# Kernel optimization log

Hardware: AMD Instinct MI355X
Metric: run time of the kernel (lower is better)

Reference implementation:

```python
import jax, jax.numpy as jnp
import numpy as np

N_NODES = 50000
N_EDGES = 800000
N_GRAPHS = 128
HEADS = 4
HDIM = 32
N_CLASSES = 10
LEAKY_ALPHA = 0.2


def setup_inputs() -> dict:
    key = jax.random.key(0)
    ks = jax.random.split(key, 12)
    src = jax.random.randint(ks[0], (N_EDGES,), 0, N_NODES, dtype=jnp.int32)
    # guarantee every node has in-degree >= 1 so 3/deg is finite
    dst_tail = jax.random.randint(ks[1], (N_EDGES - N_NODES,), 0, N_NODES, dtype=jnp.int32)
    dst = jnp.concatenate([jnp.arange(N_NODES, dtype=jnp.int32), dst_tail])
    graph_ids = jnp.sort(jax.random.randint(ks[2], (N_NODES,), 0, N_GRAPHS, dtype=jnp.int32))
    s = 0.1
    return {
        "src": src,
        "dst": dst,
        "graph_ids": graph_ids,
        "W1": jax.random.normal(ks[3], (4, HEADS * HDIM), jnp.float32) * s,
        "al1": jax.random.normal(ks[4], (HEADS, HDIM), jnp.float32) * s,
        "ar1": jax.random.normal(ks[5], (HEADS, HDIM), jnp.float32) * s,
        "W2": jax.random.normal(ks[6], (HEADS * HDIM, HEADS * HDIM), jnp.float32) * s,
        "al2": jax.random.normal(ks[7], (HEADS, HDIM), jnp.float32) * s,
        "ar2": jax.random.normal(ks[8], (HEADS, HDIM), jnp.float32) * s,
        "Wc": jax.random.normal(ks[9], (HEADS * HDIM, N_CLASSES), jnp.float32) * s,
        "bc": jax.random.normal(ks[10], (N_CLASSES,), jnp.float32) * s,
    }


def _gat_layer(x, src, dst, W, al, ar):
    # x: [N, Fin]; W: [Fin, H*D]; al, ar: [H, D]
    n = x.shape[0]
    ft = (x @ W).reshape(n, HEADS, HDIM)                       # [N, H, D]
    a1 = jnp.einsum("nhd,hd->nh", ft, al)                      # [N, H]
    a2 = jnp.einsum("nhd,hd->nh", ft, ar)                      # [N, H]
    e = jax.nn.leaky_relu(a1[src] + a2[dst], LEAKY_ALPHA)      # [E, H]
    # segment softmax over incoming edges of each dst node
    m = jax.ops.segment_max(e, dst, num_segments=n)            # [N, H]
    m = jax.lax.stop_gradient(m)
    ex = jnp.exp(e - m[dst])                                   # [E, H]
    denom = jax.ops.segment_sum(ex, dst, num_segments=n)       # [N, H]
    alpha = ex / denom[dst]                                    # [E, H]
    # gather-multiply-scatter aggregation
    out = jax.ops.segment_sum(ft[src] * alpha[:, :, None], dst, num_segments=n)  # [N, H, D]
    return jax.nn.relu(out.reshape(n, HEADS * HDIM))


def reference(src, dst, graph_ids, W1, al1, ar1, W2, al2, ar2, Wc, bc):
    n = N_NODES
    ones_e = jnp.ones(src.shape[0], jnp.float32)
    deg = jax.ops.segment_sum(ones_e, dst, num_segments=n)     # in-degrees [N]
    h = jnp.stack(
        [deg, (deg - 3.0 > 0).astype(jnp.float32), 3.0 / deg, (deg - 4.0 > 0).astype(jnp.float32)],
        axis=1,
    )                                                          # [N, 4]
    h = _gat_layer(h, src, dst, W1, al1, ar1)                  # [N, H*D]
    h = _gat_layer(h, src, dst, W2, al2, ar2)                  # [N, H*D]
    # mean_nodes: per-graph mean pooling
    gsum = jax.ops.segment_sum(h, graph_ids, num_segments=N_GRAPHS)
    cnt = jax.ops.segment_sum(jnp.ones(n, jnp.float32), graph_ids, num_segments=N_GRAPHS)
    gmean = gsum / jnp.maximum(cnt, 1.0)[:, None]              # [G, H*D]
    return jax.nn.sigmoid(gmean @ Wc + bc)                     # [G, n_classes]
```

## Files before the change

kernel.cpp:

```cpp
#include <hip/hip_runtime.h>
#include <hip/hip_fp16.h>
#include <math.h>

#define HEADS 4
#define HDIM 32
#define FDIM 128
#define NGRAPH 128
#define NCLASS 10

#define NBW 128
#define NBP 512
#define BCAP 4096
#define SLICE 4096

typedef _Float16 h4_t __attribute__((ext_vector_type(4)));
typedef float f4_t __attribute__((ext_vector_type(4)));
typedef float f2_t __attribute__((ext_vector_type(2)));

__device__ __forceinline__ float lrelu(float x) { return fmaxf(x, 0.2f * x); }

__global__ void k_wfrag(const float* __restrict__ W2, __half* __restrict__ Wfrag,
                        float* __restrict__ gsum, int* __restrict__ gcnt,
                        int* __restrict__ bcur) {
    int gid = blockIdx.x * 256 + threadIdx.x;
    ((float4*)gsum)[gid] = make_float4(0.f, 0.f, 0.f, 0.f);
    if (gid < NGRAPH) gcnt[gid] = 0;
    if (gid < NBP) bcur[gid] = 0;
    int fid = gid >> 6, l = gid & 63;
    int ks = fid >> 3, t = fid & 7;
    int k0 = ks * 16 + 4 * (l >> 4);
    int n0 = t * 16 + (l & 15);
    __half2 lo = __floats2half2_rn(W2[(k0 + 0) * FDIM + n0], W2[(k0 + 1) * FDIM + n0]);
    __half2 hi = __floats2half2_rn(W2[(k0 + 2) * FDIM + n0], W2[(k0 + 3) * FDIM + n0]);
    size_t base = ((size_t)fid * 64 + l) * 4;
    *(__half2*)(Wfrag + base)     = lo;
    *(__half2*)(Wfrag + base + 2) = hi;
}

__global__ __launch_bounds__(256) void k_part(const int* __restrict__ src,
        const int* __restrict__ dst, int E, int* __restrict__ bcur,
        unsigned int* __restrict__ part) {
    __shared__ int lcnt[NBP];
    __shared__ int loff[NBP];
    __shared__ int lpos[NBP];
    __shared__ unsigned int staged[SLICE];
    __shared__ int tgt[SLICE];
    __shared__ int ws[4];
    int tid = threadIdx.x, lane = tid & 63, w = tid >> 6;
    int beg = blockIdx.x * SLICE, end = min(E, beg + SLICE);
    int m = end - beg;
    for (int i = tid; i < NBP; i += 256) lcnt[i] = 0;
    __syncthreads();
    for (int i = beg + tid; i < end; i += 256)
        atomicAdd(&lcnt[dst[i] >> 7], 1);
    __syncthreads();
    int c0 = lcnt[2 * tid], c1 = lcnt[2 * tid + 1];
    int t = c0 + c1;
    int incl = t;
    #pragma unroll
    for (int off = 1; off < 64; off <<= 1) {
        int y = __shfl_up(incl, off);
        if (lane >= off) incl += y;
    }
    if (lane == 63) ws[w] = incl;
    __syncthreads();
    int wpre = 0;
    #pragma unroll
    for (int j = 0; j < 4; ++j) if (j < w) wpre += ws[j];
    int ex = wpre + (incl - t);
    loff[2 * tid] = ex; loff[2 * tid + 1] = ex + c0;
    if (c0) lpos[2 * tid] = atomicAdd(&bcur[2 * tid], c0);
    if (c1) lpos[2 * tid + 1] = atomicAdd(&bcur[2 * tid + 1], c1);
    lcnt[2 * tid] = 0; lcnt[2 * tid + 1] = 0;
    __syncthreads();
    for (int i = beg + tid; i < end; i += 256) {
        int s = src[i], d = dst[i];
        int b = d >> 7;
        int idx = atomicAdd(&lcnt[b], 1);
        int slot = loff[b] + idx;
        staged[slot] = ((unsigned int)(d & (NBW - 1)) << 16) | (unsigned int)s;
        tgt[slot] = b * BCAP + lpos[b] + idx;
    }
    __syncthreads();
    for (int i = tid; i < m; i += 256)
        part[tgt[i]] = staged[i];
}

__global__ __launch_bounds__(256) void k_build(const unsigned int* __restrict__ part,
        const int* __restrict__ bcur, unsigned int* __restrict__ nodeinfo,
        unsigned short* __restrict__ csr, unsigned short* __restrict__ deg16, int n) {
    __shared__ int ldeg[NBW];
    __shared__ int loffs[NBW];
    __shared__ int wtot[2];
    int b = blockIdx.x, tid = threadIdx.x;
    int lane = tid & 63, w = tid >> 6;
    if (tid < NBW) ldeg[tid] = 0;
    __syncthreads();
    int beg = b * BCAP, end = beg + bcur[b];
    for (int i = beg + tid; i < end; i += 256)
        atomicAdd(&ldeg[part[i] >> 16], 1);
    __syncthreads();
    int x = (tid < NBW) ? ldeg[tid] : 0;
    int incl = x;
    #pragma unroll
    for (int off = 1; off < 64; off <<= 1) {
        int y = __shfl_up(incl, off);
        if (lane >= off) incl += y;
    }
    if (tid < NBW && lane == 63) wtot[w] = incl;
    __syncthreads();
    if (tid < NBW) {
        int pre = incl - x;
        if (w == 1) pre += wtot[0];
        loffs[tid] = beg + pre;
        int v = b * NBW + tid;
        if (v < n) {
            nodeinfo[v] = ((unsigned int)(beg + pre) << 9) | (unsigned int)x;
            deg16[v] = (unsigned short)x;
        }
    }
    __syncthreads();
    if (tid < NBW) ldeg[tid] = 0;
    __syncthreads();
    for (int i = beg + tid; i < end; i += 256) {
        unsigned int e = part[i];
        int lv = e >> 16;
        int p = atomicAdd(&ldeg[lv], 1);
        csr[loffs[lv] + p] = (unsigned short)(e & 0xffffu);
    }
}

__global__ __launch_bounds__(256) void k_l2f(const unsigned int* __restrict__ nodeinfo,
        const unsigned short* __restrict__ csr, const unsigned short* __restrict__ deg16,
        const float* __restrict__ W1, const float* __restrict__ al1,
        const float* __restrict__ ar1, const __half* __restrict__ Wfrag,
        const float* __restrict__ al, const float* __restrict__ ar,
        unsigned char* __restrict__ ft8, float* __restrict__ a1b,
        float* __restrict__ a2b, int n) {
    __shared__ __half Alds[4][16 * 132];
    __shared__ float Slds[4][256];
    __shared__ float wla[16], wlr[16];
    int tid = threadIdx.x, l = tid & 63, w = tid >> 6;
    int c = l & 15, g = l >> 4;

    if (tid < 32) {
        int k = (tid & 15) >> 2, h = tid & 3;
        const float* av = (tid < 16) ? al1 : ar1;
        float s = 0.f;
        #pragma unroll
        for (int d = 0; d < 32; ++d) s += W1[k * FDIM + h * HDIM + d] * av[h * HDIM + d];
        if (tid < 16) wla[k * 4 + h] = s; else wlr[k * 4 + h] = s;
    }
    __syncthreads();

    int v0 = (blockIdx.x * 4 + w) * 16;

    for (int r4 = 0; r4 < 4; ++r4) {
        int v = v0 + r4 * 4 + g;
        bool vok = v < n;
        unsigned int info = vok ? nodeinfo[v] : 0;
        int beg = info >> 9;
        int dg = info & 511;
        float dv = vok ? (float)dg : 1.0f;
        float4 hvv = make_float4(dv, (dv - 3.0f > 0.0f) ? 1.0f : 0.0f, 3.0f / dv,
                                 (dv - 4.0f > 0.0f) ? 1.0f : 0.0f);
        float a2h[4];
        #pragma unroll
        for (int h = 0; h < 4; ++h)
            a2h[h] = hvv.x * wlr[0 + h] + hvv.y * wlr[4 + h] + hvv.z * wlr[8 + h] + hvv.w * wlr[12 + h];
        float P[4][4], D[4];
        #pragma unroll
        for (int h = 0; h < 4; ++h) { D[h] = 0.f;
            #pragma unroll
            for (int d = 0; d < 4; ++d) P[h][d] = 0.f; }
        for (int base2 = 0; base2 < dg; base2 += 16) {
            if (base2 + c < dg) {
                int u = csr[beg + base2 + c];
                float du = (float)deg16[u];
                float4 fu = make_float4(du, (du - 3.0f > 0.0f) ? 1.0f : 0.0f, 3.0f / du,
                                        (du - 4.0f > 0.0f) ? 1.0f : 0.0f);
                float wgt[4];
                #pragma unroll
                for (int h = 0; h < 4; ++h) {
                    float a1h = fu.x * wla[0 + h] + fu.y * wla[4 + h] + fu.z * wla[8 + h] + fu.w * wla[12 + h];
                    wgt[h] = __expf(lrelu(a1h + a2h[h]));
                }
                #pragma unroll
                for (int h = 0; h < 4; ++h) {
                    D[h] += wgt[h];
                    P[h][0] = fmaf(wgt[h], fu.x, P[h][0]);
                    P[h][1] = fmaf(wgt[h], fu.y, P[h][1]);
                    P[h][2] = fmaf(wgt[h], fu.z, P[h][2]);
                    P[h][3] = fmaf(wgt[h], fu.w, P[h][3]);
                }
            }
        }
        #pragma unroll
        for (int off = 1; off < 16; off <<= 1) {
            #pragma unroll
            for (int h = 0; h < 4; ++h) {
                D[h] += __shfl_xor(D[h], off);
                #pragma unroll
                for (int d = 0; d < 4; ++d) P[h][d] += __shfl_xor(P[h][d], off);
            }
        }
        if (vok && c == 0) {
            #pragma unroll
            for (int h = 0; h < 4; ++h) {
                float r = 1.0f / D[h];
                #pragma unroll
                for (int d = 0; d < 4; ++d)
                    Slds[w][(r4 * 4 + g) * 16 + h * 4 + d] = P[h][d] * r;
            }
        }
    }

    float2 w1c[4];
    #pragma unroll
    for (int d = 0; d < 4; ++d) w1c[d] = *(const float2*)(W1 + d * FDIM + 2 * l);
    for (int jj = 0; jj < 16; ++jj) {
        float4 s = *(const float4*)(&Slds[w][jj * 16 + g * 4]);
        float t0 = s.x * w1c[0].x + s.y * w1c[1].x + s.z * w1c[2].x + s.w * w1c[3].x;
        float t1 = s.x * w1c[0].y + s.y * w1c[1].y + s.z * w1c[2].y + s.w * w1c[3].y;
        *(__half2*)(&Alds[w][jj * 132 + 2 * l]) = __floats2half2_rn(fmaxf(t0, 0.f), fmaxf(t1, 0.f));
    }
    __syncthreads();

    f4_t acc[8];
    #pragma unroll
    for (int t = 0; t < 8; ++t) acc[t] = (f4_t){0.f, 0.f, 0.f, 0.f};
    #pragma unroll
    for (int ks = 0; ks < 8; ++ks) {
        h4_t af = *(const h4_t*)(&Alds[w][c * 132 + ks * 16 + 4 * g]);
        #pragma unroll
        for (int t = 0; t < 8; ++t) {
            h4_t bf = *(const h4_t*)(Wfrag + ((size_t)(ks * 8 + t) * 64 + l) * 4);
            acc[t] = __builtin_amdgcn_mfma_f32_16x16x16f16(af, bf, acc[t], 0, 0, 0);
        }
    }

    #pragma unroll
    for (int t = 0; t < 8; ++t) {
        #pragma unroll
        for (int r = 0; r < 4; ++r) {
            int v = v0 + 4 * g + r;
            if (v < n) {
                int pk = __builtin_amdgcn_cvt_pk_fp8_f32(acc[t][r], acc[t][r], 0, false);
                ft8[(size_t)v * FDIM + t * 16 + c] = (unsigned char)(pk & 0xff);
            }
        }
    }
    float al0[4], al1v[4], ar0[4], ar1v[4];
    #pragma unroll
    for (int h = 0; h < 4; ++h) {
        al0[h] = al[h * 32 + c]; al1v[h] = al[h * 32 + 16 + c];
        ar0[h] = ar[h * 32 + c]; ar1v[h] = ar[h * 32 + 16 + c];
    }
    #pragma unroll
    for (int r = 0; r < 4; ++r) {
        int v = v0 + 4 * g + r;
        #pragma unroll
        for (int h = 0; h < 4; ++h) {
            float p1 = acc[2 * h][r] * al0[h] + acc[2 * h + 1][r] * al1v[h];
            float p2 = acc[2 * h][r] * ar0[h] + acc[2 * h + 1][r] * ar1v[h];
            #pragma unroll
            for (int off = 1; off < 16; off <<= 1) {
                p1 += __shfl_xor(p1, off);
                p2 += __shfl_xor(p2, off);
            }
            if (c == h && v < n) {
                a1b[v * 4 + h] = p1;
                a2b[v * 4 + h] = p2;
            }
        }
    }
}

__global__ __launch_bounds__(256) void k_agg2(const unsigned int* __restrict__ nodeinfo,
        const unsigned short* __restrict__ csr, const unsigned char* __restrict__ ft8,
        const float* __restrict__ a1, const float* __restrict__ a2,
        __half* __restrict__ out, int n) {
    int tid = threadIdx.x, lane = tid & 63, w = tid >> 6;
    int qw = lane >> 4, ql = lane & 15;
    int v = blockIdx.x * 16 + w * 4 + qw;
    if (v >= n) return;
    unsigned int info = nodeinfo[v];
    int beg = info >> 9, end = beg + (info & 511);
    int h = ql >> 2;
    float a2h = a2[v * 4 + h];
    float acc[8];
    #pragma unroll
    for (int k = 0; k < 8; ++k) acc[k] = 0.f;
    float dsum = 0.f;
    const unsigned char* fbase = ft8 + (size_t)ql * 8;
    int j = beg;
    for (; j + 4 <= end; j += 4) {
        int s[4];
        #pragma unroll
        for (int k = 0; k < 4; ++k) s[k] = csr[j + k];
        float wv[4]; uint2 bv[4];
        #pragma unroll
        for (int k = 0; k < 4; ++k) {
            wv[k] = __expf(lrelu(a1[s[k] * 4 + h] + a2h));
            bv[k] = *(const uint2*)(fbase + (size_t)s[k] * FDIM);
        }
        #pragma unroll
        for (int k = 0; k < 4; ++k) {
            dsum += wv[k];
            f2_t g;
            g = __builtin_amdgcn_cvt_pk_f32_fp8(bv[k].x, false); acc[0] = fmaf(wv[k], g[0], acc[0]); acc[1] = fmaf(wv[k], g[1], acc[1]);
            g = __builtin_amdgcn_cvt_pk_f32_fp8(bv[k].x, true);  acc[2] = fmaf(wv[k], g[0], acc[2]); acc[3] = fmaf(wv[k], g[1], acc[3]);
            g = __builtin_amdgcn_cvt_pk_f32_fp8(bv[k].y, false); acc[4] = fmaf(wv[k], g[0], acc[4]); acc[5] = fmaf(wv[k], g[1], acc[5]);
            g = __builtin_amdgcn_cvt_pk_f32_fp8(bv[k].y, true);  acc[6] = fmaf(wv[k], g[0], acc[6]); acc[7] = fmaf(wv[k], g[1], acc[7]);
        }
    }
    for (; j < end; ++j) {
        int s0 = csr[j];
        float w0 = __expf(lrelu(a1[s0 * 4 + h] + a2h));
        uint2 b0 = *(const uint2*)(fbase + (size_t)s0 * FDIM);
        dsum += w0;
        f2_t g;
        g = __builtin_amdgcn_cvt_pk_f32_fp8(b0.x, false); acc[0] = fmaf(w0, g[0], acc[0]); acc[1] = fmaf(w0, g[1], acc[1]);
        g = __builtin_amdgcn_cvt_pk_f32_fp8(b0.x, true);  acc[2] = fmaf(w0, g[0], acc[2]); acc[3] = fmaf(w0, g[1], acc[3]);
        g = __builtin_amdgcn_cvt_pk_f32_fp8(b0.y, false); acc[4] = fmaf(w0, g[0], acc[4]); acc[5] = fmaf(w0, g[1], acc[5]);
        g = __builtin_amdgcn_cvt_pk_f32_fp8(b0.y, true);  acc[6] = fmaf(w0, g[0], acc[6]); acc[7] = fmaf(w0, g[1], acc[7]);
    }
    float r = 1.0f / dsum;
    __half2 o[4];
    #pragma unroll
    for (int k = 0; k < 4; ++k)
        o[k] = __floats2half2_rn(fmaxf(acc[2 * k] * r, 0.f), fmaxf(acc[2 * k + 1] * r, 0.f));
    *(float4*)(out + (size_t)v * FDIM + ql * 8) = *(float4*)o;
}

__global__ void k_pool(const __half* __restrict__ hbuf, const int* __restrict__ gid,
                       float* __restrict__ gsum, int* __restrict__ gcnt, int n) {
    const int STRIP = 32;
    int wv = (blockIdx.x * blockDim.x + threadIdx.x) >> 6;
    int lane = threadIdx.x & 63;
    int beg = wv * STRIP;
    if (beg >= n) return;
    int end = min(beg + STRIP, n);
    int f = 2 * lane;
    float2 acc = make_float2(0.f, 0.f);
    int cur = gid[beg];
    int cnt = 0;
    for (int i = beg; i < end; ++i) {
        int g = gid[i];
        if (g != cur) {
            atomicAdd(&gsum[cur * FDIM + f], acc.x);
            atomicAdd(&gsum[cur * FDIM + f + 1], acc.y);
            if (lane == 0) atomicAdd(&gcnt[cur], cnt);
            acc = make_float2(0.f, 0.f); cnt = 0; cur = g;
        }
        float2 x = __half22float2(*(const __half2*)(hbuf + (size_t)i * FDIM + f));
        acc.x += x.x; acc.y += x.y; cnt++;
    }
    atomicAdd(&gsum[cur * FDIM + f], acc.x);
    atomicAdd(&gsum[cur * FDIM + f + 1], acc.y);
    if (lane == 0) atomicAdd(&gcnt[cur], cnt);
}

__global__ void k_classify(const float* __restrict__ gsum, const int* __restrict__ gcnt,
                           const float* __restrict__ Wc, const float* __restrict__ bc,
                           float* __restrict__ out) {
    int idx = blockIdx.x * blockDim.x + threadIdx.x;
    if (idx >= NGRAPH * NCLASS) return;
    int g = idx / NCLASS, c = idx % NCLASS;
    float rc = 1.0f / fmaxf((float)gcnt[g], 1.0f);
    float s = bc[c];
    for (int k = 0; k < FDIM; ++k)
        s += gsum[g * FDIM + k] * rc * Wc[k * NCLASS + c];
    out[idx] = 1.0f / (1.0f + __expf(-s));
}

extern "C" void kernel_launch(void* const* d_in, const int* in_sizes, int n_in,
                              void* d_out, int out_size, void* d_ws, size_t ws_size,
                              hipStream_t stream) {
    const int*   src = (const int*)d_in[0];
    const int*   dst = (const int*)d_in[1];
    const int*   gid = (const int*)d_in[2];
    const float* W1  = (const float*)d_in[3];
    const float* al1 = (const float*)d_in[4];
    const float* ar1 = (const float*)d_in[5];
    const float* W2  = (const float*)d_in[6];
    const float* al2 = (const float*)d_in[7];
    const float* ar2 = (const float*)d_in[8];
    const float* Wc  = (const float*)d_in[9];
    const float* bc  = (const float*)d_in[10];
    float* out = (float*)d_out;
    const int E = in_sizes[0];
    const int N = in_sizes[2];

    char* ws = (char*)d_ws;
    size_t off = 0;
    auto alloc = [&](size_t bytes) -> void* {
        void* p = ws + off;
        off = (off + bytes + 255) & ~(size_t)255;
        return p;
    };
    unsigned int*   part = (unsigned int*)alloc((size_t)NBP * BCAP * 4);
    unsigned short* csr  = (unsigned short*)alloc((size_t)NBP * BCAP * 2);
    int*    bcur   = (int*)alloc(NBP * 4);
    unsigned int* nodeinfo = (unsigned int*)alloc((size_t)N * 4);
    unsigned short* deg16  = (unsigned short*)alloc((size_t)N * 2);
    float*  a1b    = (float*)alloc((size_t)N * HEADS * 4);
    float*  a2b    = (float*)alloc((size_t)N * HEADS * 4);
    unsigned char* ft8 = (unsigned char*)alloc((size_t)N * FDIM);
    __half* hbuf   = (__half*)alloc((size_t)N * FDIM * 2);
    __half* Wfrag  = (__half*)alloc((size_t)FDIM * FDIM * 2);
    float*  gsum   = (float*)alloc((size_t)NGRAPH * FDIM * 4);
    int*    gcnt   = (int*)alloc((size_t)NGRAPH * 4);

    int pb_edges = (E + SLICE - 1) / SLICE;
    int nb2 = (N + NBW - 1) / NBW;

    k_wfrag<<<16, 256, 0, stream>>>(W2, Wfrag, gsum, gcnt, bcur);
    k_part<<<pb_edges, 256, 0, stream>>>(src, dst, E, bcur, part);
    k_build<<<nb2, 256, 0, stream>>>(part, bcur, nodeinfo, csr, deg16, N);
    k_l2f<<<(N + 63) / 64, 256, 0, stream>>>(nodeinfo, csr, deg16, W1, al1, ar1,
                                             Wfrag, al2, ar2, ft8, a1b, a2b, N);
    k_agg2<<<(N + 15) / 16, 256, 0, stream>>>(nodeinfo, csr, ft8, a1b, a2b, hbuf, N);

    int pb = (((N + 31) / 32) + 3) / 4;
    k_pool<<<pb, 256, 0, stream>>>(hbuf, gid, gsum, gcnt, N);
    k_classify<<<(NGRAPH * NCLASS + 255) / 256, 256, 0, stream>>>(gsum, gcnt, Wc, bc, out);
}
```

Before: 121.4 us.

## Split layer-1 aggregation into its own kernel with one node per 16-lane group

The fused layer-1 aggregation plus layer-2 MFMA projection kernel is split in two. The new aggregation kernel gives each 16-lane group a single node across more blocks, and writes the 16 normalized feature sums per node to a global buffer. The projection kernel then reads those sums instead of shared memory. This is meant to raise parallelism and occupancy for the irregular gather phase and free the MFMA kernel from serial per-node loops, at the cost of an extra launch and a round trip of 64 bytes per node through global memory.

```diff
diff --git a/kernel.cpp b/kernel.cpp
--- a/kernel.cpp
+++ b/kernel.cpp
@@ -130,96 +130,94 @@
     }
 }
 
-__global__ __launch_bounds__(256) void k_l2f(const unsigned int* __restrict__ nodeinfo,
+__global__ __launch_bounds__(256) void k_agg1(const unsigned int* __restrict__ nodeinfo,
         const unsigned short* __restrict__ csr, const unsigned short* __restrict__ deg16,
         const float* __restrict__ W1, const float* __restrict__ al1,
-        const float* __restrict__ ar1, const __half* __restrict__ Wfrag,
+        const float* __restrict__ ar1, float* __restrict__ Sbuf, int n) {
+    __shared__ float wla[16], wlr[16];
+    int tid = threadIdx.x;
+    if (tid < 32) {
+        int k = (tid & 15) >> 2, h = tid & 3;
+        const float* av = (tid < 16) ? al1 : ar1;
+        float s = 0.f;
+        #pragma unroll
+        for (int d = 0; d < 32; ++d) s += W1[k * FDIM + h * HDIM + d] * av[h * HDIM + d];
+        if (tid < 16) wla[k * 4 + h] = s; else wlr[k * 4 + h] = s;
+    }
+    __syncthreads();
+    int c = tid & 15;
+    int v = blockIdx.x * 16 + (tid >> 4);
+    if (v >= n) return;
+    unsigned int info = nodeinfo[v];
+    int beg = info >> 9;
+    int dg = info & 511;
+    float dv = (float)dg;
+    float4 hvv = make_float4(dv, (dv - 3.0f > 0.0f) ? 1.0f : 0.0f, 3.0f / dv,
+                             (dv - 4.0f > 0.0f) ? 1.0f : 0.0f);
+    float a2h[4];
+    #pragma unroll
+    for (int h = 0; h < 4; ++h)
+        a2h[h] = hvv.x * wlr[0 + h] + hvv.y * wlr[4 + h] + hvv.z * wlr[8 + h] + hvv.w * wlr[12 + h];
+    float P[4][4], D[4];
+    #pragma unroll
+    for (int h = 0; h < 4; ++h) { D[h] = 0.f;
+        #pragma unroll
+        for (int d = 0; d < 4; ++d) P[h][d] = 0.f; }
+    for (int j = beg + c; j < beg + dg; j += 16) {
+        int u = csr[j];
+        float du = (float)deg16[u];
+        float4 fu = make_float4(du, (du - 3.0f > 0.0f) ? 1.0f : 0.0f, 3.0f / du,
+                                (du - 4.0f > 0.0f) ? 1.0f : 0.0f);
+        float wgt[4];
+        #pragma unroll
+        for (int h = 0; h < 4; ++h) {
+            float a1h = fu.x * wla[0 + h] + fu.y * wla[4 + h] + fu.z * wla[8 + h] + fu.w * wla[12 + h];
+            wgt[h] = __expf(lrelu(a1h + a2h[h]));
+        }
+        #pragma unroll
+        for (int h = 0; h < 4; ++h) {
+            D[h] += wgt[h];
+            P[h][0] = fmaf(wgt[h], fu.x, P[h][0]);
+            P[h][1] = fmaf(wgt[h], fu.y, P[h][1]);
+            P[h][2] = fmaf(wgt[h], fu.z, P[h][2]);
+            P[h][3] = fmaf(wgt[h], fu.w, P[h][3]);
+        }
+    }
+    #pragma unroll
+    for (int off = 1; off < 16; off <<= 1) {
+        #pragma unroll
+        for (int h = 0; h < 4; ++h) {
+            D[h] += __shfl_xor(D[h], off);
+            #pragma unroll
+            for (int d = 0; d < 4; ++d) P[h][d] += __shfl_xor(P[h][d], off);
+        }
+    }
+    if (c == 0) {
+        #pragma unroll
+        for (int h = 0; h < 4; ++h) {
+            float r = 1.0f / D[h];
+            *(float4*)(Sbuf + v * 16 + h * 4) =
+                make_float4(P[h][0] * r, P[h][1] * r, P[h][2] * r, P[h][3] * r);
+        }
+    }
+}
+
+__global__ __launch_bounds__(256) void k_layer2(const float* __restrict__ Sbuf,
+        const float* __restrict__ W1, const __half* __restrict__ Wfrag,
         const float* __restrict__ al, const float* __restrict__ ar,
         unsigned char* __restrict__ ft8, float* __restrict__ a1b,
         float* __restrict__ a2b, int n) {
     __shared__ __half Alds[4][16 * 132];
-    __shared__ float Slds[4][256];
-    __shared__ float wla[16], wlr[16];
     int tid = threadIdx.x, l = tid & 63, w = tid >> 6;
     int c = l & 15, g = l >> 4;
-
-    if (tid < 32) {
-        int k = (tid & 15) >> 2, h = tid & 3;
-        const float* av = (tid < 16) ? al1 : ar1;
-        float s = 0.f;
-        #pragma unroll
-        for (int d = 0; d < 32; ++d) s += W1[k * FDIM + h * HDIM + d] * av[h * HDIM + d];
-        if (tid < 16) wla[k * 4 + h] = s; else wlr[k * 4 + h] = s;
-    }
-    __syncthreads();
-
     int v0 = (blockIdx.x * 4 + w) * 16;
-
-    for (int r4 = 0; r4 < 4; ++r4) {
-        int v = v0 + r4 * 4 + g;
-        bool vok = v < n;
-        unsigned int info = vok ? nodeinfo[v] : 0;
-        int beg = info >> 9;
-        int dg = info & 511;
-        float dv = vok ? (float)dg : 1.0f;
-        float4 hvv = make_float4(dv, (dv - 3.0f > 0.0f) ? 1.0f : 0.0f, 3.0f / dv,
-                                 (dv - 4.0f > 0.0f) ? 1.0f : 0.0f);
-        float a2h[4];
-        #pragma unroll
-        for (int h = 0; h < 4; ++h)
-            a2h[h] = hvv.x * wlr[0 + h] + hvv.y * wlr[4 + h] + hvv.z * wlr[8 + h] + hvv.w * wlr[12 + h];
-        float P[4][4], D[4];
-        #pragma unroll
-        for (int h = 0; h < 4; ++h) { D[h] = 0.f;
-            #pragma unroll
-            for (int d = 0; d < 4; ++d) P[h][d] = 0.f; }
-        for (int base2 = 0; base2 < dg; base2 += 16) {
-            if (base2 + c < dg) {
-                int u = csr[beg + base2 + c];
-                float du = (float)deg16[u];
-                float4 fu = make_float4(du, (du - 3.0f > 0.0f) ? 1.0f : 0.0f, 3.0f / du,
-                                        (du - 4.0f > 0.0f) ? 1.0f : 0.0f);
-                float wgt[4];
-                #pragma unroll
-                for (int h = 0; h < 4; ++h) {
-                    float a1h = fu.x * wla[0 + h] + fu.y * wla[4 + h] + fu.z * wla[8 + h] + fu.w * wla[12 + h];
-                    wgt[h] = __expf(lrelu(a1h + a2h[h]));
-                }
-                #pragma unroll
-                for (int h = 0; h < 4; ++h) {
-                    D[h] += wgt[h];
-                    P[h][0] = fmaf(wgt[h], fu.x, P[h][0]);
-                    P[h][1] = fmaf(wgt[h], fu.y, P[h][1]);
-                    P[h][2] = fmaf(wgt[h], fu.z, P[h][2]);
-                    P[h][3] = fmaf(wgt[h], fu.w, P[h][3]);
-                }
-            }
-        }
-        #pragma unroll
-        for (int off = 1; off < 16; off <<= 1) {
-            #pragma unroll
-            for (int h = 0; h < 4; ++h) {
-                D[h] += __shfl_xor(D[h], off);
-                #pragma unroll
-                for (int d = 0; d < 4; ++d) P[h][d] += __shfl_xor(P[h][d], off);
-            }
-        }
-        if (vok && c == 0) {
-            #pragma unroll
-            for (int h = 0; h < 4; ++h) {
-                float r = 1.0f / D[h];
-                #pragma unroll
-                for (int d = 0; d < 4; ++d)
-                    Slds[w][(r4 * 4 + g) * 16 + h * 4 + d] = P[h][d] * r;
-            }
-        }
-    }
 
     float2 w1c[4];
     #pragma unroll
     for (int d = 0; d < 4; ++d) w1c[d] = *(const float2*)(W1 + d * FDIM + 2 * l);
     for (int jj = 0; jj < 16; ++jj) {
-        float4 s = *(const float4*)(&Slds[w][jj * 16 + g * 4]);
+        int v = min(v0 + jj, n - 1);
+        float4 s = *(const float4*)(Sbuf + (size_t)v * 16 + g * 4);
         float t0 = s.x * w1c[0].x + s.y * w1c[1].x + s.z * w1c[2].x + s.w * w1c[3].x;
         float t1 = s.x * w1c[0].y + s.y * w1c[1].y + s.z * w1c[2].y + s.w * w1c[3].y;
         *(__half2*)(&Alds[w][jj * 132 + 2 * l]) = __floats2half2_rn(fmaxf(t0, 0.f), fmaxf(t1, 0.f));
@@ -404,6 +402,7 @@
     int*    bcur   = (int*)alloc(NBP * 4);
     unsigned int* nodeinfo = (unsigned int*)alloc((size_t)N * 4);
     unsigned short* deg16  = (unsigned short*)alloc((size_t)N * 2);
+    float*  Sbuf   = (float*)alloc((size_t)N * 16 * 4);
     float*  a1b    = (float*)alloc((size_t)N * HEADS * 4);
     float*  a2b    = (float*)alloc((size_t)N * HEADS * 4);
     unsigned char* ft8 = (unsigned char*)alloc((size_t)N * FDIM);
@@ -418,8 +417,8 @@
     k_wfrag<<<16, 256, 0, stream>>>(W2, Wfrag, gsum, gcnt, bcur);
     k_part<<<pb_edges, 256, 0, stream>>>(src, dst, E, bcur, part);
     k_build<<<nb2, 256, 0, stream>>>(part, bcur, nodeinfo, csr, deg16, N);
-    k_l2f<<<(N + 63) / 64, 256, 0, stream>>>(nodeinfo, csr, deg16, W1, al1, ar1,
-                                             Wfrag, al2, ar2, ft8, a1b, a2b, N);
+    k_agg1<<<(N + 15) / 16, 256, 0, stream>>>(nodeinfo, csr, deg16, W1, al1, ar1, Sbuf, N);
+    k_layer2<<<(N + 63) / 64, 256, 0, stream>>>(Sbuf, W1, Wfrag, al2, ar2, ft8, a1b, a2b, N);
     k_agg2<<<(N + 15) / 16, 256, 0, stream>>>(nodeinfo, csr, ft8, a1b, a2b, hbuf, N);
 
     int pb = (((N + 31) / 32) + 3) / 4;
```

New measurement: 119.5 us. No clear change (-1.5%).
